# Performance work log

Hardware: AMD Instinct MI355X
Metric: run time of the kernel (lower is better)

Reference implementation:

```python
import jax, jax.numpy as jnp
import numpy as np

DIM = 768
GP_NUM = 49


def setup_inputs() -> dict:
    key = jax.random.key(0)
    ks = jax.random.split(key, 7)
    b, n, d = 16, 1024, DIM
    s = d ** -0.5
    x = jax.random.normal(ks[0], (b, n, d), dtype=jnp.float32)
    W_qkv = jax.random.normal(ks[1], (d, 3 * d), dtype=jnp.float32) * s
    b_qkv = jnp.zeros((3 * d,), dtype=jnp.float32)
    W_proj = jax.random.normal(ks[2], (d, d), dtype=jnp.float32) * s
    b_proj = jnp.zeros((d,), dtype=jnp.float32)
    W_gp = jax.random.normal(ks[3], (d, GP_NUM), dtype=jnp.float32) * s
    alpha = jnp.zeros((1,), dtype=jnp.float32)
    return {"x": x, "W_qkv": W_qkv, "b_qkv": b_qkv, "W_proj": W_proj,
            "b_proj": b_proj, "W_gp": W_gp, "alpha": alpha}


def reference(x, W_qkv, b_qkv, W_proj, b_proj, W_gp, alpha):
    d = x.shape[-1]
    scale = d ** -0.5
    qkv = x @ W_qkv + b_qkv                      # (b, n, 3d)
    q, k, v = jnp.split(qkv, 3, axis=-1)
    scores = jnp.einsum('bnd,bmd->bnm', q, k) * scale
    attn = jax.nn.softmax(scores, axis=-1)       # (b, n, n)
    gw = jax.nn.softmax(q @ W_gp, axis=-1)       # (b, n, gp_num)
    group = jnp.einsum('bng,bmg->bnm', gw, gw)   # (b, n, n)
    a = jax.nn.sigmoid(alpha)                    # (1,)
    weights = attn * (a + (1.0 - a) * group)
    out = jnp.einsum('bnm,bmd->bnd', weights, v)
    return out @ W_proj + b_proj
```

## Files before the change

### kernel.cpp

```cpp
#include <hip/hip_runtime.h>
#include <stdint.h>

typedef __attribute__((ext_vector_type(8))) short short8;
typedef __attribute__((ext_vector_type(4))) short short4v;
typedef __attribute__((ext_vector_type(4))) float floatx4;
typedef _Float16 half2v __attribute__((ext_vector_type(2)));

__device__ __forceinline__ float b2f(unsigned short u) {
  union { unsigned int i; float f; } v; v.i = ((unsigned int)u) << 16; return v.f;
}
__device__ __forceinline__ unsigned short f2b(float f) {
  union { float f; unsigned int i; } v; v.f = f;
  unsigned int i = v.i;
  return (unsigned short)((i + 0x7FFFu + ((i >> 16) & 1u)) >> 16);
}
__device__ __forceinline__ short4v pack4(float a, float b, float c, float d) {
  short4v r;
  r[0] = (short)f2b(a); r[1] = (short)f2b(b); r[2] = (short)f2b(c); r[3] = (short)f2b(d);
  return r;
}

__device__ __forceinline__ void stage16(const unsigned short* g, unsigned short* lds_base) {
  __builtin_amdgcn_global_load_lds((__attribute__((address_space(1))) const unsigned int*)g,
                                   (__attribute__((address_space(3))) unsigned int*)lds_base,
                                   16, 0, 0);
}

template<int SYT, int SXT>
__global__ __launch_bounds__(256, 4) void gemm_bt(
    const unsigned short* __restrict__ A, const unsigned short* __restrict__ B,
    unsigned short* __restrict__ Cb, float* __restrict__ Cf,
    const float* __restrict__ rowdiv, const float* __restrict__ bias,
    int K, int lda, int ldb, int ldc,
    long long sA, long long sB, long long sC, long long sRD)
{
  const int tid  = threadIdx.x;
  const int lane = tid & 63;
  const int wave = tid >> 6;
  const int wr = wave >> 1, wc = wave & 1;
  int m0, n0;
  if constexpr (SYT > 0) {
    const int lin  = blockIdx.x;
    const int xcd  = lin & 7;
    const int rem  = lin >> 3;
    const int yloc = rem / SXT;
    const int x    = rem - yloc * SXT;
    m0 = (xcd * SYT + yloc) * 128;
    n0 = x * 128;
  } else {
    m0 = blockIdx.y * 128;
    n0 = blockIdx.x * 128;
  }
  const int bz = blockIdx.z;
  A += (long long)bz * sA;
  B += (long long)bz * sB;
  const float* rd = rowdiv ? rowdiv + (long long)bz * sRD : (const float*)0;

  __shared__ unsigned short As[128 * 32];
  __shared__ unsigned short Bs[128 * 32];

  floatx4 acc[4][4];
#pragma unroll
  for (int i = 0; i < 4; ++i)
#pragma unroll
    for (int j = 0; j < 4; ++j) acc[i][j] = floatx4{0.f, 0.f, 0.f, 0.f};

  const int t    = (lane & 7) ^ (lane >> 3);
  const int srow = 2 * (lane >> 3) + (t >> 2);
  const int scol = (t & 3) * 8;
  const unsigned short* ga0 = A + (long long)(m0 + wave * 32 + srow) * lda + scol;
  const unsigned short* ga1 = ga0 + 16LL * lda;
  const unsigned short* gb0 = B + (long long)(n0 + wave * 32 + srow) * ldb + scol;
  const unsigned short* gb1 = gb0 + 16LL * ldb;
  unsigned short* lA0 = As + wave * 1024;
  unsigned short* lA1 = lA0 + 512;
  unsigned short* lB0 = Bs + wave * 1024;
  unsigned short* lB1 = lB0 + 512;

  const int l15  = lane & 15;
  const int q    = lane >> 4;
  const int rofs = (l15 >> 1) * 64 + (((q + 4 * (l15 & 1)) ^ (l15 >> 1)) * 8);

  for (int kt = 0; kt < K; kt += 32) {
    __syncthreads();
    stage16(ga0 + kt, lA0);
    stage16(ga1 + kt, lA1);
    stage16(gb0 + kt, lB0);
    stage16(gb1 + kt, lB1);
    __syncthreads();
    short8 af[4], bfv[4];
#pragma unroll
    for (int i = 0; i < 4; ++i) af[i]  = *(const short8*)&As[(wr * 32 + i * 8) * 64 + rofs];
#pragma unroll
    for (int j = 0; j < 4; ++j) bfv[j] = *(const short8*)&Bs[(wc * 32 + j * 8) * 64 + rofs];
#pragma unroll
    for (int i = 0; i < 4; ++i)
#pragma unroll
      for (int j = 0; j < 4; ++j)
        acc[i][j] = __builtin_amdgcn_mfma_f32_16x16x32_bf16(bfv[j], af[i], acc[i][j], 0, 0, 0);
  }

#pragma unroll
  for (int i = 0; i < 4; ++i) {
    const int row = m0 + wr * 64 + i * 16 + l15;
    const float rcp = rd ? __builtin_amdgcn_rcpf(rd[row]) : 1.0f;
#pragma unroll
    for (int j = 0; j < 4; ++j) {
      const int colb = n0 + wc * 64 + j * 16 + q * 4;
      floatx4 v = acc[i][j];
      if (rd) { v[0] *= rcp; v[1] *= rcp; v[2] *= rcp; v[3] *= rcp; }
      if (bias) {
        const float4 bi = *(const float4*)&bias[colb];
        v[0] += bi.x; v[1] += bi.y; v[2] += bi.z; v[3] += bi.w;
      }
      if (Cb) *(short4v*)&Cb[(long long)bz * sC + (long long)row * ldc + colb] = pack4(v[0], v[1], v[2], v[3]);
      else    *(floatx4*)&Cf[(long long)bz * sC + (long long)row * ldc + colb] = v;
    }
  }
}

__global__ __launch_bounds__(256) void score_weights(
    const unsigned short* __restrict__ qkv, const unsigned short* __restrict__ gw,
    unsigned short* __restrict__ Wout, float* __restrict__ L,
    const float* __restrict__ alpha)
{
  const int tid  = threadIdx.x;
  const int lane = tid & 63;
  const int wave = tid >> 6;
  const int wr = wave >> 1, wc = wave & 1;
  const int bx = blockIdx.x;
  const int by = blockIdx.y;
  const int m0 = ((bx >> 1) * 2 + (by >> 2)) * 128;
  const int n0 = ((bx & 1) * 4 + (by & 3)) * 128;
  const int b  = blockIdx.z;

  const int l15 = lane & 15;
  const int q   = lane >> 4;
  const int q8  = q * 8;

  const unsigned short* gq = gw + ((long long)(b * 1024 + m0 + wr * 64)) * 64;
  const unsigned short* gk = gw + ((long long)(b * 1024 + n0 + wc * 64)) * 64;
  floatx4 gacc[4][4];
#pragma unroll
  for (int i = 0; i < 4; ++i)
#pragma unroll
    for (int j = 0; j < 4; ++j) gacc[i][j] = floatx4{0.f, 0.f, 0.f, 0.f};
#pragma unroll
  for (int ks = 0; ks < 2; ++ks) {
    short8 af[4], bfv[4];
#pragma unroll
    for (int i = 0; i < 4; ++i) af[i]  = *(const short8*)&gq[(long long)(i * 16 + l15) * 64 + ks * 32 + q8];
#pragma unroll
    for (int j = 0; j < 4; ++j) bfv[j] = *(const short8*)&gk[(long long)(j * 16 + l15) * 64 + ks * 32 + q8];
#pragma unroll
    for (int i = 0; i < 4; ++i)
#pragma unroll
      for (int j = 0; j < 4; ++j)
        gacc[i][j] = __builtin_amdgcn_mfma_f32_16x16x32_bf16(bfv[j], af[i], gacc[i][j], 0, 0, 0);
  }
  const float aa    = 1.0f / (1.0f + __expf(-alpha[0]));
  const float onema = 1.0f - aa;
  half2v gfp[4][4][2];
#pragma unroll
  for (int i = 0; i < 4; ++i)
#pragma unroll
    for (int j = 0; j < 4; ++j) {
      gfp[i][j][0] = half2v{(_Float16)(aa + onema * gacc[i][j][0]),
                            (_Float16)(aa + onema * gacc[i][j][1])};
      gfp[i][j][1] = half2v{(_Float16)(aa + onema * gacc[i][j][2]),
                            (_Float16)(aa + onema * gacc[i][j][3])};
    }

  const unsigned short* Aq = qkv + ((long long)(b * 1024 + m0)) * 1536;
  const unsigned short* Bk = qkv + ((long long)(b * 1024 + n0)) * 1536 + 768;

  __shared__ unsigned short As[128 * 32];
  __shared__ unsigned short Bs[128 * 32];

  floatx4 sacc[4][4];
#pragma unroll
  for (int i = 0; i < 4; ++i)
#pragma unroll
    for (int j = 0; j < 4; ++j) sacc[i][j] = floatx4{0.f, 0.f, 0.f, 0.f};

  const int t    = (lane & 7) ^ (lane >> 3);
  const int srow = 2 * (lane >> 3) + (t >> 2);
  const int scol = (t & 3) * 8;
  const unsigned short* ga0 = Aq + (long long)(wave * 32 + srow) * 1536 + scol;
  const unsigned short* ga1 = ga0 + 16LL * 1536;
  const unsigned short* gb0 = Bk + (long long)(wave * 32 + srow) * 1536 + scol;
  const unsigned short* gb1 = gb0 + 16LL * 1536;
  unsigned short* lA0 = As + wave * 1024;
  unsigned short* lA1 = lA0 + 512;
  unsigned short* lB0 = Bs + wave * 1024;
  unsigned short* lB1 = lB0 + 512;

  const int rofs = (l15 >> 1) * 64 + (((q + 4 * (l15 & 1)) ^ (l15 >> 1)) * 8);

  for (int kt = 0; kt < 768; kt += 32) {
    __syncthreads();
    stage16(ga0 + kt, lA0);
    stage16(ga1 + kt, lA1);
    stage16(gb0 + kt, lB0);
    stage16(gb1 + kt, lB1);
    __syncthreads();
    short8 af[4], bfv[4];
#pragma unroll
    for (int i = 0; i < 4; ++i) af[i]  = *(const short8*)&As[(wr * 32 + i * 8) * 64 + rofs];
#pragma unroll
    for (int j = 0; j < 4; ++j) bfv[j] = *(const short8*)&Bs[(wc * 32 + j * 8) * 64 + rofs];
#pragma unroll
    for (int i = 0; i < 4; ++i)
#pragma unroll
      for (int j = 0; j < 4; ++j)
        sacc[i][j] = __builtin_amdgcn_mfma_f32_16x16x32_bf16(bfv[j], af[i], sacc[i][j], 0, 0, 0);
  }

  const float scale = 0.03608439182435161f;
  unsigned short* Wb = Wout + ((long long)b << 20);

#pragma unroll
  for (int i = 0; i < 4; ++i) {
    const int row = m0 + wr * 64 + i * 16 + l15;
    float ls = 0.0f;
#pragma unroll
    for (int j = 0; j < 4; ++j) {
      const int colb = n0 + wc * 64 + j * 16 + q * 4;
      float e0 = __expf(sacc[i][j][0] * scale);
      float e1 = __expf(sacc[i][j][1] * scale);
      float e2 = __expf(sacc[i][j][2] * scale);
      float e3 = __expf(sacc[i][j][3] * scale);
      ls += (e0 + e1) + (e2 + e3);
      *(short4v*)&Wb[(long long)row * 1024 + colb] =
        pack4(e0 * (float)gfp[i][j][0][0], e1 * (float)gfp[i][j][0][1],
              e2 * (float)gfp[i][j][1][0], e3 * (float)gfp[i][j][1][1]);
    }
    ls += __shfl_xor(ls, 16, 64);
    ls += __shfl_xor(ls, 32, 64);
    if (lane < 16) atomicAdd(&L[b * 1024 + row], ls);
  }
}

__global__ __launch_bounds__(256) void gw_mfma(
    const unsigned short* __restrict__ qkv, const unsigned short* __restrict__ Wgp64,
    unsigned short* __restrict__ gw, float* __restrict__ L)
{
  const int lane = threadIdx.x & 63;
  const int wave = threadIdx.x >> 6;
  const int l15  = lane & 15;
  const int q    = lane >> 4;
  const int q8   = q * 8;
  const long long row0 = (long long)blockIdx.x * 64 + wave * 16;
  const unsigned short* A = qkv + row0 * 1536;

  if (q == 0) L[row0 + l15] = 0.0f;

  floatx4 acc[4];
#pragma unroll
  for (int j = 0; j < 4; ++j) acc[j] = floatx4{0.f, 0.f, 0.f, 0.f};

  for (int kt = 0; kt < 768; kt += 32) {
    short8 af = *(const short8*)&A[(long long)l15 * 1536 + kt + q8];
    short8 bf[4];
#pragma unroll
    for (int j = 0; j < 4; ++j)
      bf[j] = *(const short8*)&Wgp64[(j * 16 + l15) * 768 + kt + q8];
#pragma unroll
    for (int j = 0; j < 4; ++j)
      acc[j] = __builtin_amdgcn_mfma_f32_16x16x32_bf16(bf[j], af, acc[j], 0, 0, 0);
  }

  float mx = -1e30f;
#pragma unroll
  for (int j = 0; j < 4; ++j)
#pragma unroll
    for (int e = 0; e < 4; ++e) {
      const int col = j * 16 + q * 4 + e;
      if (col < 49) mx = fmaxf(mx, acc[j][e]);
    }
  mx = fmaxf(mx, __shfl_xor(mx, 16, 64));
  mx = fmaxf(mx, __shfl_xor(mx, 32, 64));

  float ev[4][4];
  float s = 0.0f;
#pragma unroll
  for (int j = 0; j < 4; ++j)
#pragma unroll
    for (int e = 0; e < 4; ++e) {
      const int col = j * 16 + q * 4 + e;
      const float x = (col < 49) ? __expf(acc[j][e] - mx) : 0.0f;
      ev[j][e] = x;
      s += x;
    }
  s += __shfl_xor(s, 16, 64);
  s += __shfl_xor(s, 32, 64);
  const float inv = 1.0f / s;

  unsigned short* out = gw + (row0 + l15) * 64;
#pragma unroll
  for (int j = 0; j < 4; ++j)
    *(short4v*)&out[j * 16 + q * 4] =
      pack4(ev[j][0] * inv, ev[j][1] * inv, ev[j][2] * inv, ev[j][3] * inv);
}

__global__ __launch_bounds__(256) void small_gemm_nt(
    const unsigned short* __restrict__ A, const unsigned short* __restrict__ B,
    unsigned short* __restrict__ C)
{
  const int lane = threadIdx.x & 63;
  const int wave = threadIdx.x >> 6;
  const int l15  = lane & 15;
  const int q    = lane >> 4;
  const int q8   = q * 8;
  const int rows0 = (blockIdx.y * 4 + wave) * 16;
  const int cols0 = blockIdx.x * 64;

  floatx4 acc[4];
#pragma unroll
  for (int j = 0; j < 4; ++j) acc[j] = floatx4{0.f, 0.f, 0.f, 0.f};

  for (int kt = 0; kt < 768; kt += 32) {
    short8 af = *(const short8*)&A[(rows0 + l15) * 768 + kt + q8];
    short8 bf[4];
#pragma unroll
    for (int j = 0; j < 4; ++j)
      bf[j] = *(const short8*)&B[(cols0 + j * 16 + l15) * 768 + kt + q8];
#pragma unroll
    for (int j = 0; j < 4; ++j)
      acc[j] = __builtin_amdgcn_mfma_f32_16x16x32_bf16(bf[j], af, acc[j], 0, 0, 0);
  }

  unsigned short* out = C + (rows0 + l15) * 768 + cols0;
#pragma unroll
  for (int j = 0; j < 4; ++j)
    *(short4v*)&out[j * 16 + q * 4] = pack4(acc[j][0], acc[j][1], acc[j][2], acc[j][3]);
}

__global__ void convert_f2b(const float* __restrict__ in, unsigned short* __restrict__ out, long long n)
{
  const long long stride = (long long)gridDim.x * blockDim.x * 8;
  for (long long i = ((long long)blockIdx.x * blockDim.x + threadIdx.x) * 8; i < n; i += stride) {
    const float4 a = *(const float4*)(in + i);
    const float4 b = *(const float4*)(in + i + 4);
    short8 r;
    r[0] = (short)f2b(a.x); r[1] = (short)f2b(a.y); r[2] = (short)f2b(a.z); r[3] = (short)f2b(a.w);
    r[4] = (short)f2b(b.x); r[5] = (short)f2b(b.y); r[6] = (short)f2b(b.z); r[7] = (short)f2b(b.w);
    *(short8*)(out + i) = r;
  }
}

__global__ void transpose_f2b(const float* __restrict__ in, unsigned short* __restrict__ out,
                              int R, int C, int ldin, int ldout, int Rpad)
{
  __shared__ unsigned short t[32][33];
  const int c0 = blockIdx.x * 32, r0 = blockIdx.y * 32;
  for (int i = threadIdx.y; i < 32; i += 8) {
    const int r = r0 + i, c = c0 + threadIdx.x;
    if (r < R && c < C) t[i][threadIdx.x] = f2b(in[(long long)r * ldin + c]);
  }
  __syncthreads();
  for (int i = threadIdx.y; i < 32; i += 8) {
    const int r = c0 + i, c = r0 + threadIdx.x;
    if (r < Rpad && c < R) {
      unsigned short v = 0;
      if (r < C) v = t[threadIdx.x][i];
      out[(long long)r * ldout + c] = v;
    }
  }
}

__global__ void slice_f2b(const float* __restrict__ in, unsigned short* __restrict__ out)
{
  const long long idx = (long long)blockIdx.x * 256 + threadIdx.x;
  const int r = (int)(idx / 768), c = (int)(idx - (long long)r * 768);
  out[idx] = f2b(in[(long long)r * 2304 + 1536 + c]);
}

__global__ __launch_bounds__(256) void bias2_kernel(
    const unsigned short* __restrict__ WprojT, const float* __restrict__ b_qkv,
    const float* __restrict__ b_proj, float* __restrict__ bias2)
{
  const int lane = threadIdx.x & 63;
  const int wave = threadIdx.x >> 6;
  const int j = blockIdx.x * 4 + wave;
  float s = 0.0f;
#pragma unroll
  for (int tt = 0; tt < 12; ++tt) {
    const int d = tt * 64 + lane;
    s += b2f(WprojT[j * 768 + d]) * b_qkv[1536 + d];
  }
#pragma unroll
  for (int m = 1; m < 64; m <<= 1) s += __shfl_xor(s, m, 64);
  if (lane == 0) bias2[j] = b_proj[j] + s;
}

extern "C" void kernel_launch(void* const* d_in, const int* in_sizes, int n_in,
                              void* d_out, int out_size, void* d_ws, size_t ws_size,
                              hipStream_t stream)
{
  const float* x      = (const float*)d_in[0];
  const float* W_qkv  = (const float*)d_in[1];
  const float* b_qkv  = (const float*)d_in[2];
  const float* W_proj = (const float*)d_in[3];
  const float* b_proj = (const float*)d_in[4];
  const float* W_gp   = (const float*)d_in[5];
  const float* alpha  = (const float*)d_in[6];

  char* p = (char*)d_ws;
  auto alloc = [&](size_t bytes) { char* r = p; p += (bytes + 255) & ~255ULL; return r; };
  unsigned short* qk     = (unsigned short*)alloc(16384ULL * 1536 * 2);
  unsigned short* xb     = (unsigned short*)alloc(16384ULL * 768 * 2);
  unsigned short* WqkvT  = (unsigned short*)alloc(1536ULL * 768 * 2);
  unsigned short* WprojT = (unsigned short*)alloc(768ULL * 768 * 2);
  unsigned short* WvB    = (unsigned short*)alloc(768ULL * 768 * 2);
  unsigned short* Wcomb  = (unsigned short*)alloc(768ULL * 768 * 2);
  unsigned short* Wgp64  = (unsigned short*)alloc(64ULL * 768 * 2);
  unsigned short* gwbuf  = (unsigned short*)alloc(16384ULL * 64 * 2);
  float*          Lbuf   = (float*)alloc(16384ULL * 4);
  float*          bias2  = (float*)alloc(768ULL * 4);
  unsigned short* wmat   = (unsigned short*)alloc(16ULL * 1024 * 1024 * 2);
  unsigned short* vpT    = (unsigned short*)alloc(16ULL * 768 * 1024 * 2);

  const dim3 blk256(256);
  const dim3 tb(32, 8);

  convert_f2b<<<dim3(2048), blk256, 0, stream>>>(x, xb, 16384LL * 768);
  transpose_f2b<<<dim3(48, 24), tb, 0, stream>>>(W_qkv, WqkvT, 768, 1536, 2304, 768, 1536);
  transpose_f2b<<<dim3(24, 24), tb, 0, stream>>>(W_proj, WprojT, 768, 768, 768, 768, 768);
  transpose_f2b<<<dim3(2, 24), tb, 0, stream>>>(W_gp, Wgp64, 768, 49, 49, 768, 64);
  slice_f2b<<<dim3(2304), blk256, 0, stream>>>(W_qkv, WvB);
  small_gemm_nt<<<dim3(12, 12), blk256, 0, stream>>>(WprojT, WvB, Wcomb);
  bias2_kernel<<<dim3(192), blk256, 0, stream>>>(WprojT, b_qkv, b_proj, bias2);

  gemm_bt<16, 12><<<dim3(1536, 1, 1), blk256, 0, stream>>>(xb, WqkvT, qk, (float*)0,
                                                           (const float*)0, b_qkv,
                                                           768, 768, 768, 1536, 0, 0, 0, 0);

  gw_mfma<<<dim3(256), blk256, 0, stream>>>(qk, Wgp64, gwbuf, Lbuf);

  score_weights<<<dim3(8, 8, 16), blk256, 0, stream>>>(qk, gwbuf, wmat, Lbuf, alpha);

  gemm_bt<0, 0><<<dim3(8, 6, 16), blk256, 0, stream>>>(Wcomb, xb, vpT, (float*)0,
                                                       (const float*)0, (const float*)0,
                                                       768, 768, 768, 1024,
                                                       0, 1024LL * 768, 768LL * 1024, 0);

  gemm_bt<0, 0><<<dim3(6, 8, 16), blk256, 0, stream>>>(wmat, vpT, (unsigned short*)0, (float*)d_out,
                                                       Lbuf, bias2,
                                                       1024, 1024, 1024, 768,
                                                       1024LL * 1024, 768LL * 1024, 1024LL * 768, 1024);
}
```

Baseline: 360.9 us.

## Merge prep kernels into one launch and co-schedule QKV and V-projection GEMMs

Replaces seven small preprocessing launches (convert, three transposes, slice, small GEMM, bias) with one block-indexed prep kernel that reads fp32 weights directly, dropping the WprojT and WvB intermediates. The QKV projection GEMM and the Wcomb·x V-projection GEMM are merged into a single launch whose blocks branch by index, and the final GEMM becomes a dedicated kernel. The aim is to cut launch overhead and tail idling between dependent small launches. In exchange the XCD-aware block remapping of the QKV GEMM is lost, and the fused Wcomb GEMM now does strided uncoalesced fp32 loads of W_proj.

```diff
diff --git a/kernel.cpp b/kernel.cpp
--- a/kernel.cpp
+++ b/kernel.cpp
@@ -26,38 +26,17 @@
                                    16, 0, 0);
 }
 
-template<int SYT, int SXT>
-__global__ __launch_bounds__(256, 4) void gemm_bt(
+__device__ __forceinline__ void gemm128_core(
+    unsigned short* As, unsigned short* Bs,
     const unsigned short* __restrict__ A, const unsigned short* __restrict__ B,
     unsigned short* __restrict__ Cb, float* __restrict__ Cf,
-    const float* __restrict__ rowdiv, const float* __restrict__ bias,
-    int K, int lda, int ldb, int ldc,
-    long long sA, long long sB, long long sC, long long sRD)
+    const float* __restrict__ rd, const float* __restrict__ bias,
+    int K, int lda, int ldb, int ldc, int m0, int n0)
 {
   const int tid  = threadIdx.x;
   const int lane = tid & 63;
   const int wave = tid >> 6;
   const int wr = wave >> 1, wc = wave & 1;
-  int m0, n0;
-  if constexpr (SYT > 0) {
-    const int lin  = blockIdx.x;
-    const int xcd  = lin & 7;
-    const int rem  = lin >> 3;
-    const int yloc = rem / SXT;
-    const int x    = rem - yloc * SXT;
-    m0 = (xcd * SYT + yloc) * 128;
-    n0 = x * 128;
-  } else {
-    m0 = blockIdx.y * 128;
-    n0 = blockIdx.x * 128;
-  }
-  const int bz = blockIdx.z;
-  A += (long long)bz * sA;
-  B += (long long)bz * sB;
-  const float* rd = rowdiv ? rowdiv + (long long)bz * sRD : (const float*)0;
-
-  __shared__ unsigned short As[128 * 32];
-  __shared__ unsigned short Bs[128 * 32];
 
   floatx4 acc[4][4];
 #pragma unroll
@@ -113,10 +92,49 @@
         const float4 bi = *(const float4*)&bias[colb];
         v[0] += bi.x; v[1] += bi.y; v[2] += bi.z; v[3] += bi.w;
       }
-      if (Cb) *(short4v*)&Cb[(long long)bz * sC + (long long)row * ldc + colb] = pack4(v[0], v[1], v[2], v[3]);
-      else    *(floatx4*)&Cf[(long long)bz * sC + (long long)row * ldc + colb] = v;
-    }
-  }
+      if (Cb) *(short4v*)&Cb[(long long)row * ldc + colb] = pack4(v[0], v[1], v[2], v[3]);
+      else    *(floatx4*)&Cf[(long long)row * ldc + colb] = v;
+    }
+  }
+}
+
+__global__ __launch_bounds__(256, 4) void fused_mid(
+    const unsigned short* __restrict__ xb, const unsigned short* __restrict__ WqkvT,
+    const unsigned short* __restrict__ Wcomb,
+    unsigned short* __restrict__ qk, unsigned short* __restrict__ vpT,
+    const float* __restrict__ b_qkv)
+{
+  __shared__ unsigned short As[128 * 32];
+  __shared__ unsigned short Bs[128 * 32];
+  const int x  = blockIdx.x;
+  const int bz = blockIdx.z;
+  if (x < 96) {
+    const int m0 = (bz * 8 + (x & 7)) * 128;
+    const int n0 = (x >> 3) * 128;
+    gemm128_core(As, Bs, xb, WqkvT, qk, (float*)0, (const float*)0, b_qkv,
+                 768, 768, 768, 1536, m0, n0);
+  } else {
+    const int a  = x - 96;
+    const int m0 = (a >> 3) * 128;
+    const int n0 = (a & 7) * 128;
+    gemm128_core(As, Bs, Wcomb, xb + (long long)bz * 1024 * 768,
+                 vpT + (long long)bz * 768 * 1024, (float*)0,
+                 (const float*)0, (const float*)0,
+                 768, 768, 768, 1024, m0, n0);
+  }
+}
+
+__global__ __launch_bounds__(256, 4) void gemm_final(
+    const unsigned short* __restrict__ wmat, const unsigned short* __restrict__ vpT,
+    float* __restrict__ out, const float* __restrict__ L, const float* __restrict__ bias2)
+{
+  __shared__ unsigned short As[128 * 32];
+  __shared__ unsigned short Bs[128 * 32];
+  const int bz = blockIdx.z;
+  gemm128_core(As, Bs, wmat + (long long)bz * 1024 * 1024, vpT + (long long)bz * 768 * 1024,
+               (unsigned short*)0, out + (long long)bz * 1024 * 768,
+               L + bz * 1024, bias2,
+               1024, 1024, 1024, 768, blockIdx.y * 128, blockIdx.x * 128);
 }
 
 __global__ __launch_bounds__(256) void score_weights(
@@ -303,95 +321,107 @@
       pack4(ev[j][0] * inv, ev[j][1] * inv, ev[j][2] * inv, ev[j][3] * inv);
 }
 
-__global__ __launch_bounds__(256) void small_gemm_nt(
-    const unsigned short* __restrict__ A, const unsigned short* __restrict__ B,
-    unsigned short* __restrict__ C)
-{
-  const int lane = threadIdx.x & 63;
-  const int wave = threadIdx.x >> 6;
-  const int l15  = lane & 15;
-  const int q    = lane >> 4;
-  const int q8   = q * 8;
-  const int rows0 = (blockIdx.y * 4 + wave) * 16;
-  const int cols0 = blockIdx.x * 64;
-
-  floatx4 acc[4];
-#pragma unroll
-  for (int j = 0; j < 4; ++j) acc[j] = floatx4{0.f, 0.f, 0.f, 0.f};
-
-  for (int kt = 0; kt < 768; kt += 32) {
-    short8 af = *(const short8*)&A[(rows0 + l15) * 768 + kt + q8];
-    short8 bf[4];
+__global__ __launch_bounds__(256) void prep(
+    const float* __restrict__ x, const float* __restrict__ W_qkv,
+    const float* __restrict__ b_qkv, const float* __restrict__ W_proj,
+    const float* __restrict__ b_proj, const float* __restrict__ W_gp,
+    unsigned short* __restrict__ xb, unsigned short* __restrict__ WqkvT,
+    unsigned short* __restrict__ Wgp64, unsigned short* __restrict__ Wcomb,
+    float* __restrict__ bias2)
+{
+  __shared__ unsigned short tsh[32][33];
+  const int blk = blockIdx.x;
+  const int tid = threadIdx.x;
+
+  if (blk < 2048) {
+    const long long n = 16384LL * 768;
+    const long long stride = 2048LL * 256 * 8;
+    for (long long i = ((long long)blk * 256 + tid) * 8; i < n; i += stride) {
+      const float4 a = *(const float4*)(x + i);
+      const float4 b = *(const float4*)(x + i + 4);
+      short8 r;
+      r[0] = (short)f2b(a.x); r[1] = (short)f2b(a.y); r[2] = (short)f2b(a.z); r[3] = (short)f2b(a.w);
+      r[4] = (short)f2b(b.x); r[5] = (short)f2b(b.y); r[6] = (short)f2b(b.z); r[7] = (short)f2b(b.w);
+      *(short8*)(xb + i) = r;
+    }
+  } else if (blk < 3248) {
+    const float* in; unsigned short* out; int R, C, ldin, ldout, Rpad, bx, by;
+    if (blk < 3200) {
+      const int idx = blk - 2048;
+      in = W_qkv; out = WqkvT; R = 768; C = 1536; ldin = 2304; ldout = 768; Rpad = 1536;
+      bx = idx % 48; by = idx / 48;
+    } else {
+      const int idx = blk - 3200;
+      in = W_gp; out = Wgp64; R = 768; C = 49; ldin = 49; ldout = 768; Rpad = 64;
+      bx = idx % 2; by = idx / 2;
+    }
+    const int tx = tid & 31, ty = tid >> 5;
+    const int c0 = bx * 32, r0 = by * 32;
+    for (int i = ty; i < 32; i += 8) {
+      const int r = r0 + i, c = c0 + tx;
+      if (r < R && c < C) tsh[i][tx] = f2b(in[(long long)r * ldin + c]);
+    }
+    __syncthreads();
+    for (int i = ty; i < 32; i += 8) {
+      const int r = c0 + i, c = r0 + tx;
+      if (r < Rpad && c < R) {
+        unsigned short v = 0;
+        if (r < C) v = tsh[tx][i];
+        out[(long long)r * ldout + c] = v;
+      }
+    }
+  } else if (blk < 3392) {
+    const int idx  = blk - 3248;
+    const int lane = tid & 63;
+    const int wave = tid >> 6;
+    const int l15  = lane & 15;
+    const int q    = lane >> 4;
+    const int q8   = q * 8;
+    const int cols0 = (idx % 12) * 64;
+    const int rows0 = ((idx / 12) * 4 + wave) * 16;
+
+    floatx4 acc[4];
+#pragma unroll
+    for (int j = 0; j < 4; ++j) acc[j] = floatx4{0.f, 0.f, 0.f, 0.f};
+
+    for (int kt = 0; kt < 768; kt += 32) {
+      short8 af;
+#pragma unroll
+      for (int u = 0; u < 8; ++u)
+        af[u] = (short)f2b(W_proj[(long long)(kt + q8 + u) * 768 + rows0 + l15]);
+      short8 bf[4];
+#pragma unroll
+      for (int j = 0; j < 4; ++j) {
+        const float* brow = W_qkv + (long long)(cols0 + j * 16 + l15) * 2304 + 1536 + kt + q8;
+        const float4 b0 = *(const float4*)brow;
+        const float4 b1 = *(const float4*)(brow + 4);
+        bf[j][0] = (short)f2b(b0.x); bf[j][1] = (short)f2b(b0.y);
+        bf[j][2] = (short)f2b(b0.z); bf[j][3] = (short)f2b(b0.w);
+        bf[j][4] = (short)f2b(b1.x); bf[j][5] = (short)f2b(b1.y);
+        bf[j][6] = (short)f2b(b1.z); bf[j][7] = (short)f2b(b1.w);
+      }
+#pragma unroll
+      for (int j = 0; j < 4; ++j)
+        acc[j] = __builtin_amdgcn_mfma_f32_16x16x32_bf16(bf[j], af, acc[j], 0, 0, 0);
+    }
+    unsigned short* out = Wcomb + (long long)(rows0 + l15) * 768 + cols0;
 #pragma unroll
     for (int j = 0; j < 4; ++j)
-      bf[j] = *(const short8*)&B[(cols0 + j * 16 + l15) * 768 + kt + q8];
-#pragma unroll
-    for (int j = 0; j < 4; ++j)
-      acc[j] = __builtin_amdgcn_mfma_f32_16x16x32_bf16(bf[j], af, acc[j], 0, 0, 0);
-  }
-
-  unsigned short* out = C + (rows0 + l15) * 768 + cols0;
-#pragma unroll
-  for (int j = 0; j < 4; ++j)
-    *(short4v*)&out[j * 16 + q * 4] = pack4(acc[j][0], acc[j][1], acc[j][2], acc[j][3]);
-}
-
-__global__ void convert_f2b(const float* __restrict__ in, unsigned short* __restrict__ out, long long n)
-{
-  const long long stride = (long long)gridDim.x * blockDim.x * 8;
-  for (long long i = ((long long)blockIdx.x * blockDim.x + threadIdx.x) * 8; i < n; i += stride) {
-    const float4 a = *(const float4*)(in + i);
-    const float4 b = *(const float4*)(in + i + 4);
-    short8 r;
-    r[0] = (short)f2b(a.x); r[1] = (short)f2b(a.y); r[2] = (short)f2b(a.z); r[3] = (short)f2b(a.w);
-    r[4] = (short)f2b(b.x); r[5] = (short)f2b(b.y); r[6] = (short)f2b(b.z); r[7] = (short)f2b(b.w);
-    *(short8*)(out + i) = r;
-  }
-}
-
-__global__ void transpose_f2b(const float* __restrict__ in, unsigned short* __restrict__ out,
-                              int R, int C, int ldin, int ldout, int Rpad)
-{
-  __shared__ unsigned short t[32][33];
-  const int c0 = blockIdx.x * 32, r0 = blockIdx.y * 32;
-  for (int i = threadIdx.y; i < 32; i += 8) {
-    const int r = r0 + i, c = c0 + threadIdx.x;
-    if (r < R && c < C) t[i][threadIdx.x] = f2b(in[(long long)r * ldin + c]);
-  }
-  __syncthreads();
-  for (int i = threadIdx.y; i < 32; i += 8) {
-    const int r = c0 + i, c = r0 + threadIdx.x;
-    if (r < Rpad && c < R) {
-      unsigned short v = 0;
-      if (r < C) v = t[threadIdx.x][i];
-      out[(long long)r * ldout + c] = v;
-    }
-  }
-}
-
-__global__ void slice_f2b(const float* __restrict__ in, unsigned short* __restrict__ out)
-{
-  const long long idx = (long long)blockIdx.x * 256 + threadIdx.x;
-  const int r = (int)(idx / 768), c = (int)(idx - (long long)r * 768);
-  out[idx] = f2b(in[(long long)r * 2304 + 1536 + c]);
-}
-
-__global__ __launch_bounds__(256) void bias2_kernel(
-    const unsigned short* __restrict__ WprojT, const float* __restrict__ b_qkv,
-    const float* __restrict__ b_proj, float* __restrict__ bias2)
-{
-  const int lane = threadIdx.x & 63;
-  const int wave = threadIdx.x >> 6;
-  const int j = blockIdx.x * 4 + wave;
-  float s = 0.0f;
-#pragma unroll
-  for (int tt = 0; tt < 12; ++tt) {
-    const int d = tt * 64 + lane;
-    s += b2f(WprojT[j * 768 + d]) * b_qkv[1536 + d];
-  }
-#pragma unroll
-  for (int m = 1; m < 64; m <<= 1) s += __shfl_xor(s, m, 64);
-  if (lane == 0) bias2[j] = b_proj[j] + s;
+      *(short4v*)&out[j * 16 + q * 4] = pack4(acc[j][0], acc[j][1], acc[j][2], acc[j][3]);
+  } else {
+    const int lane = tid & 63;
+    const int wave = tid >> 6;
+    const int j = (blk - 3392) * 4 + wave;
+    float s = 0.0f;
+#pragma unroll
+    for (int tt = 0; tt < 12; ++tt) {
+      const int d = tt * 64 + lane;
+      s += W_proj[(long long)d * 768 + j] * b_qkv[1536 + d];
+    }
+#pragma unroll
+    for (int m = 1; m < 64; m <<= 1) s += __shfl_xor(s, m, 64);
+    if (lane == 0) bias2[j] = b_proj[j] + s;
+  }
 }
 
 extern "C" void kernel_launch(void* const* d_in, const int* in_sizes, int n_in,
@@ -411,8 +441,6 @@
   unsigned short* qk     = (unsigned short*)alloc(16384ULL * 1536 * 2);
   unsigned short* xb     = (unsigned short*)alloc(16384ULL * 768 * 2);
   unsigned short* WqkvT  = (unsigned short*)alloc(1536ULL * 768 * 2);
-  unsigned short* WprojT = (unsigned short*)alloc(768ULL * 768 * 2);
-  unsigned short* WvB    = (unsigned short*)alloc(768ULL * 768 * 2);
   unsigned short* Wcomb  = (unsigned short*)alloc(768ULL * 768 * 2);
   unsigned short* Wgp64  = (unsigned short*)alloc(64ULL * 768 * 2);
   unsigned short* gwbuf  = (unsigned short*)alloc(16384ULL * 64 * 2);
@@ -422,31 +450,15 @@
   unsigned short* vpT    = (unsigned short*)alloc(16ULL * 768 * 1024 * 2);
 
   const dim3 blk256(256);
-  const dim3 tb(32, 8);
-
-  convert_f2b<<<dim3(2048), blk256, 0, stream>>>(x, xb, 16384LL * 768);
-  transpose_f2b<<<dim3(48, 24), tb, 0, stream>>>(W_qkv, WqkvT, 768, 1536, 2304, 768, 1536);
-  transpose_f2b<<<dim3(24, 24), tb, 0, stream>>>(W_proj, WprojT, 768, 768, 768, 768, 768);
-  transpose_f2b<<<dim3(2, 24), tb, 0, stream>>>(W_gp, Wgp64, 768, 49, 49, 768, 64);
-  slice_f2b<<<dim3(2304), blk256, 0, stream>>>(W_qkv, WvB);
-  small_gemm_nt<<<dim3(12, 12), blk256, 0, stream>>>(WprojT, WvB, Wcomb);
-  bias2_kernel<<<dim3(192), blk256, 0, stream>>>(WprojT, b_qkv, b_proj, bias2);
-
-  gemm_bt<16, 12><<<dim3(1536, 1, 1), blk256, 0, stream>>>(xb, WqkvT, qk, (float*)0,
-                                                           (const float*)0, b_qkv,
-                                                           768, 768, 768, 1536, 0, 0, 0, 0);
+
+  prep<<<dim3(3584), blk256, 0, stream>>>(x, W_qkv, b_qkv, W_proj, b_proj, W_gp,
+                                          xb, WqkvT, Wgp64, Wcomb, bias2);
+
+  fused_mid<<<dim3(144, 1, 16), blk256, 0, stream>>>(xb, WqkvT, Wcomb, qk, vpT, b_qkv);
 
   gw_mfma<<<dim3(256), blk256, 0, stream>>>(qk, Wgp64, gwbuf, Lbuf);
 
   score_weights<<<dim3(8, 8, 16), blk256, 0, stream>>>(qk, gwbuf, wmat, Lbuf, alpha);
 
-  gemm_bt<0, 0><<<dim3(8, 6, 16), blk256, 0, stream>>>(Wcomb, xb, vpT, (float*)0,
-                                                       (const float*)0, (const float*)0,
-                                                       768, 768, 768, 1024,
-                                                       0, 1024LL * 768, 768LL * 1024, 0);
-
-  gemm_bt<0, 0><<<dim3(6, 8, 16), blk256, 0, stream>>>(wmat, vpT, (unsigned short*)0, (float*)d_out,
-                                                       Lbuf, bias2,
-                                                       1024, 1024, 1024, 768,
-                                                       1024LL * 1024, 768LL * 1024, 1024LL * 768, 1024);
-}
+  gemm_final<<<dim3(6, 8, 16), blk256, 0, stream>>>(wmat, vpT, (float*)d_out, Lbuf, bias2);
+}
```

New measurement: 398.5 us. 10.4% more time.
